# Optimization experiments

Measured on AMD Instinct MI355X. Metric: run time of the kernel, lower is better.

Reference implementation:

```python
import jax, jax.numpy as jnp
import numpy as np

N = 30000        # nodes
E = 150000       # edges
IN = 16          # in_feats
H = 32           # hidden_feats
C = 10           # num_classes


def setup_inputs() -> dict:
    key = jax.random.key(0)
    ks = jax.random.split(key, 11)
    s = 0.05
    return {
        "x": jax.random.normal(ks[0], (N, IN), jnp.float32),
        "edge_attr": jax.random.normal(ks[1], (E, 1), jnp.float32),
        "W1": jax.random.normal(ks[2], (1, IN * H), jnp.float32) * s,
        "b1": jax.random.normal(ks[3], (IN * H,), jnp.float32) * s,
        "W2": jax.random.normal(ks[4], (IN * H, IN * H), jnp.float32) * s,
        "b2": jax.random.normal(ks[5], (IN * H,), jnp.float32) * s,
        "root": jax.random.normal(ks[6], (IN, H), jnp.float32) * s,
        "bias1": jax.random.normal(ks[7], (H,), jnp.float32) * s,
        "Wg": jax.random.normal(ks[8], (H, C), jnp.float32) * s,
        "bg": jax.random.normal(ks[9], (C,), jnp.float32) * s,
        "edge_index": jax.random.randint(ks[10], (2, E), 0, N),
    }


def _forward(x, edge_attr, W1, b1, W2, b2, root, bias1, Wg, bg, edge_index):
    src, dst = edge_index[0], edge_index[1]

    # ---- NNConv: edge-MLP generates per-edge [IN, H] weight matrices ----
    h = jax.nn.relu(edge_attr @ W1 + b1)          # [E, IN*H]
    theta = (h @ W2 + b2).reshape(E, IN, H)       # [E, IN, H]
    msg = jnp.einsum('ei,eio->eo', x[src], theta)  # per-edge matvec [E, H]
    summed = jax.ops.segment_sum(msg, dst, num_segments=N)            # [N, H]
    cnt = jax.ops.segment_sum(jnp.ones((E,), x.dtype), dst, num_segments=N)
    aggr = summed / jnp.maximum(cnt, 1.0)[:, None]  # mean aggregation
    h1 = aggr + x @ root + bias1                    # root weight + bias
    h1 = jax.nn.relu(h1)
    # dropout skipped (eval mode)

    # ---- GCNConv with self-loops and symmetric normalization ----
    xw = h1 @ Wg                                   # [N, C]
    loop = jnp.arange(N)
    row = jnp.concatenate([src, loop])
    col = jnp.concatenate([dst, loop])
    deg = jax.ops.segment_sum(jnp.ones(row.shape, x.dtype), col, num_segments=N)
    dinv = jnp.where(deg > 0, jax.lax.rsqrt(jnp.maximum(deg, 1e-12)), 0.0)
    norm = dinv[row] * dinv[col]                   # [E+N]
    out = jax.ops.segment_sum(xw[row] * norm[:, None], col, num_segments=N) + bg

    return jax.nn.log_softmax(out, axis=1)


def reference(x, edge_attr, W1, b1, W2, b2, root, bias1, Wg, bg, edge_index):
    return _forward(x, edge_attr, W1, b1, W2, b2, root, bias1, Wg, bg, edge_index)
```

## Files before the change

### kernel.cpp

```cpp
#include <hip/hip_runtime.h>
#include <math.h>

#define N_NODES 30000
#define N_EDGES 150000
#define NB_E ((N_EDGES + 255) / 256)

__device__ __forceinline__ unsigned bf16_rne(float f) {
    unsigned u = __float_as_uint(f);
    u += 0x7FFFu + ((u >> 16) & 1u);
    return u >> 16;
}

__global__ void k1z_rank(const float* __restrict__ W1, const float* __restrict__ b1,
                         float* __restrict__ tsort, int* __restrict__ ksort,
                         int* __restrict__ deg) {
    __shared__ float st[512];
    int tid = threadIdx.x;
    float w = W1[tid], b = b1[tid];
    float t = (w != 0.0f) ? (-b / w) : 3.0e38f;
    st[tid] = t;
    __syncthreads();
    int rank = 0;
#pragma unroll 8
    for (int j = 0; j < 512; ++j) {
        float tj = st[j];
        rank += (tj < t || (tj == t && j < tid)) ? 1 : 0;
    }
    tsort[rank] = t;
    ksort[rank] = tid;
    int4* dz = (int4*)deg;
    for (int i = tid; i < N_NODES / 4; i += 512) dz[i] = make_int4(0, 0, 0, 0);
}

__global__ void __launch_bounds__(256) f2_prep(
        const int* __restrict__ ei, const float* __restrict__ ea,
        const float* __restrict__ tsort,
        int* __restrict__ deg, int* __restrict__ rankm,
        const float* __restrict__ W1, const float* __restrict__ b1,
        const float* __restrict__ W2, const int* __restrict__ ksort,
        float* __restrict__ PbA, float* __restrict__ PbB,
        float* __restrict__ SA, float* __restrict__ SB) {
    if (blockIdx.x < NB_E) {
        __shared__ float ts[512];
        for (int i = threadIdx.x; i < 512; i += 256) ts[i] = tsort[i];
        __syncthreads();
        int e = blockIdx.x * 256 + threadIdx.x;
        if (e >= N_EDGES) return;
        int rank = atomicAdd(&deg[ei[N_EDGES + e]], 1);
        float a = ea[e];
        int lo = 0, hi = 512;
        while (lo < hi) {
            int mid = (lo + hi) >> 1;
            if (ts[mid] < a) lo = mid + 1; else hi = mid;
        }
        rankm[e] = (rank << 10) | lo;
    } else {
        int bb = blockIdx.x - NB_E;
        int c = bb & 31;
        int jc = bb >> 5;
        int jt = jc * 256 + threadIdx.x;
        int jsrc = ((jt & 15) << 5) | (jt >> 4);
        float ba = 0.0f, bb2 = 0.0f, sa = 0.0f, sb = 0.0f;
#pragma unroll 4
        for (int s = 0; s < 16; ++s) {
            int k = c * 16 + s;
            float w = W1[k], b = b1[k];
            bool act = (w < 0.0f) || (w == 0.0f && b > 0.0f);
            if (act) {
                float w2 = W2[k * 512 + jsrc];
                ba = fmaf(w, w2, ba);
                bb2 = fmaf(b, w2, bb2);
            }
            int kr = ksort[c * 16 + s];
            float wr = W1[kr], br = b1[kr];
            float sgn = (wr > 0.0f) ? 1.0f : ((wr < 0.0f) ? -1.0f : 0.0f);
            float w2r = W2[kr * 512 + jsrc];
            sa = fmaf(sgn * wr, w2r, sa);
            sb = fmaf(sgn * br, w2r, sb);
        }
        PbA[c * 512 + jt] = ba; PbB[c * 512 + jt] = bb2;
        SA[c * 512 + jt] = sa;  SB[c * 512 + jt] = sb;
    }
}

__global__ void __launch_bounds__(1024) f3_scan_emit(
        const int* __restrict__ deg, int* __restrict__ offs,
        const float* __restrict__ W1, const float* __restrict__ b1,
        const float* __restrict__ b2, const float* __restrict__ W2,
        const int* __restrict__ ksort,
        const float* __restrict__ PbA, const float* __restrict__ PbB,
        const float* __restrict__ SA, const float* __restrict__ SB,
        unsigned int* __restrict__ T) {
    __shared__ int part[1024];
    if (blockIdx.x == 0) {
        int t = threadIdx.x;
        int base = t * 30;
        int loc[30];
        int s = 0;
#pragma unroll
        for (int i = 0; i < 30; ++i) {
            int idx = base + i;
            int v = (idx < N_NODES) ? deg[idx] : 0;
            loc[i] = v;
            s += v;
        }
        part[t] = s;
        __syncthreads();
        for (int off = 1; off < 1024; off <<= 1) {
            int v = part[t];
            int add = (t >= off) ? part[t - off] : 0;
            __syncthreads();
            part[t] = v + add;
            __syncthreads();
        }
        int run = (t > 0) ? part[t - 1] : 0;
#pragma unroll
        for (int i = 0; i < 30; ++i) {
            int idx = base + i;
            if (idx < N_NODES) offs[idx] = run;
            run += loc[i];
        }
        if (t == 1023) offs[N_NODES] = run;
    } else {
        int c = (blockIdx.x - 1) * 2 + (threadIdx.x >> 9);
        int jt = threadIdx.x & 511;
        int jsrc = ((jt & 15) << 5) | (jt >> 4);
        float runA = 0.0f, runB = 0.0f;
#pragma unroll
        for (int c2 = 0; c2 < 32; ++c2) {
            runA += PbA[c2 * 512 + jt];
            runB += PbB[c2 * 512 + jt];
            if (c2 < c) { runA += SA[c2 * 512 + jt]; runB += SB[c2 * 512 + jt]; }
        }
        float bb2 = b2[jsrc];
#pragma unroll 4
        for (int s = 0; s < 16; ++s) {
            int m = c * 16 + s;
            T[m * 512 + jt] = (bf16_rne(runA) << 16) | bf16_rne(runB + bb2);
            int k = ksort[m];
            float w = W1[k], b = b1[k];
            float sgn = (w > 0.0f) ? 1.0f : ((w < 0.0f) ? -1.0f : 0.0f);
            float w2 = W2[k * 512 + jsrc];
            runA = fmaf(sgn * w, w2, runA);
            runB = fmaf(sgn * b, w2, runB);
        }
        if (c == 31) {
            T[512 * 512 + jt] = (bf16_rne(runA) << 16) | bf16_rne(runB + bb2);
        }
    }
}

__global__ void __launch_bounds__(256) k3_edges(
        const float* __restrict__ x, const float* __restrict__ ea,
        const int* __restrict__ ei, const int* __restrict__ rankm,
        const int* __restrict__ offs, const unsigned int* __restrict__ T,
        unsigned short* __restrict__ msgbuf, int* __restrict__ ssrc) {
    int gid = blockIdx.x * blockDim.x + threadIdx.x;
    int lane = gid & 31;
    int g = gid >> 5;
    int e0 = g << 1;
    if (e0 >= N_EDGES) return;
    float2 aa = *(const float2*)(ea + e0);
    int2 ss = *(const int2*)(ei + e0);
    int2 dd = *(const int2*)(ei + N_EDGES + e0);
    int2 rr = *(const int2*)(rankm + e0);
    int m0 = rr.x & 1023, m1 = rr.y & 1023;
    int slot0 = offs[dd.x] + (rr.x >> 10);
    int slot1 = offs[dd.y] + (rr.y >> 10);
    const uint4* T0 = (const uint4*)(T + m0 * 512 + lane * 16);
    const uint4* T1 = (const uint4*)(T + m1 * 512 + lane * 16);
    uint4 p0 = T0[0], p1 = T0[1], p2 = T0[2], p3 = T0[3];
    uint4 q0 = T1[0], q1 = T1[1], q2 = T1[2], q3 = T1[3];
    float xv0 = (lane < 16) ? x[ss.x * 16 + lane] : 0.0f;
    float xv1 = (lane < 16) ? x[ss.y * 16 + lane] : 0.0f;
    float xa0 = 0.0f, xb0 = 0.0f, xa1 = 0.0f, xb1 = 0.0f;
    float xi;
#define STEP2(w0, w1, i)                                                   \
    xi = __shfl(xv0, i, 32);                                               \
    xa0 = fmaf(xi, __uint_as_float((w0) & 0xFFFF0000u), xa0);              \
    xb0 = fmaf(xi, __uint_as_float((w0) << 16), xb0);                      \
    xi = __shfl(xv1, i, 32);                                               \
    xa1 = fmaf(xi, __uint_as_float((w1) & 0xFFFF0000u), xa1);              \
    xb1 = fmaf(xi, __uint_as_float((w1) << 16), xb1);
    STEP2(p0.x, q0.x, 0)  STEP2(p0.y, q0.y, 1)  STEP2(p0.z, q0.z, 2)  STEP2(p0.w, q0.w, 3)
    STEP2(p1.x, q1.x, 4)  STEP2(p1.y, q1.y, 5)  STEP2(p1.z, q1.z, 6)  STEP2(p1.w, q1.w, 7)
    STEP2(p2.x, q2.x, 8)  STEP2(p2.y, q2.y, 9)  STEP2(p2.z, q2.z, 10) STEP2(p2.w, q2.w, 11)
    STEP2(p3.x, q3.x, 12) STEP2(p3.y, q3.y, 13) STEP2(p3.z, q3.z, 14) STEP2(p3.w, q3.w, 15)
#undef STEP2
    float msg0 = fmaf(aa.x, xa0, xb0);
    float msg1 = fmaf(aa.y, xa1, xb1);
    msgbuf[slot0 * 32 + lane] = (unsigned short)bf16_rne(msg0);
    msgbuf[slot1 * 32 + lane] = (unsigned short)bf16_rne(msg1);
    if (lane == 0) { ssrc[slot0] = ss.x; ssrc[slot1] = ss.y; }
}

__global__ void k4_nodes(const float* __restrict__ x, const int* __restrict__ offs,
                         const unsigned int* __restrict__ msgbuf,
                         const float* __restrict__ root, const float* __restrict__ bias1,
                         const float* __restrict__ Wg,
                         float* __restrict__ xw12) {
    __shared__ float sroot[512], sb1[32], swg[320];
    for (int i = threadIdx.x; i < 512; i += blockDim.x) sroot[i] = root[i];
    for (int i = threadIdx.x; i < 32; i += blockDim.x) sb1[i] = bias1[i];
    for (int i = threadIdx.x; i < 320; i += blockDim.x) swg[i] = Wg[i];
    __syncthreads();
    int n = blockIdx.x * blockDim.x + threadIdx.x;
    if (n >= N_NODES) return;
    int s0 = offs[n], s1 = offs[n + 1];
    float agg[32];
#pragma unroll
    for (int o = 0; o < 32; ++o) agg[o] = 0.0f;
    for (int sl = s0; sl < s1; ++sl) {
        const uint4* rp = (const uint4*)(msgbuf + sl * 16);
#pragma unroll
        for (int q = 0; q < 4; ++q) {
            uint4 v = rp[q];
            agg[q * 8 + 0] += __uint_as_float(v.x << 16);
            agg[q * 8 + 1] += __uint_as_float(v.x & 0xFFFF0000u);
            agg[q * 8 + 2] += __uint_as_float(v.y << 16);
            agg[q * 8 + 3] += __uint_as_float(v.y & 0xFFFF0000u);
            agg[q * 8 + 4] += __uint_as_float(v.z << 16);
            agg[q * 8 + 5] += __uint_as_float(v.z & 0xFFFF0000u);
            agg[q * 8 + 6] += __uint_as_float(v.w << 16);
            agg[q * 8 + 7] += __uint_as_float(v.w & 0xFFFF0000u);
        }
    }
    float c = (float)(s1 - s0);
    float inv = 1.0f / fmaxf(c, 1.0f);
    const float4* xp = (const float4*)(x + n * 16);
    float xr[16];
#pragma unroll
    for (int q = 0; q < 4; ++q) {
        float4 v = xp[q];
        xr[q * 4 + 0] = v.x; xr[q * 4 + 1] = v.y;
        xr[q * 4 + 2] = v.z; xr[q * 4 + 3] = v.w;
    }
    float acc[10];
#pragma unroll
    for (int cc = 0; cc < 10; ++cc) acc[cc] = 0.0f;
#pragma unroll
    for (int o = 0; o < 32; ++o) {
        float h = agg[o] * inv + sb1[o];
#pragma unroll
        for (int i = 0; i < 16; ++i) h = fmaf(xr[i], sroot[i * 32 + o], h);
        h = fmaxf(h, 0.0f);
#pragma unroll
        for (int cc = 0; cc < 10; ++cc) acc[cc] = fmaf(h, swg[o * 10 + cc], acc[cc]);
    }
    float4* op = (float4*)(xw12 + n * 12);
    op[0] = make_float4(acc[0], acc[1], acc[2], acc[3]);
    op[1] = make_float4(acc[4], acc[5], acc[6], acc[7]);
    op[2] = make_float4(acc[8], acc[9], rsqrtf(c + 1.0f), 0.0f);
}

__global__ void k56_final(const int* __restrict__ offs, const int* __restrict__ ssrc,
                          const float* __restrict__ xw12,
                          const float* __restrict__ bg, float* __restrict__ out) {
    __shared__ float sbg[16];
    if (threadIdx.x < 10) sbg[threadIdx.x] = bg[threadIdx.x];
    __syncthreads();
    int n = blockIdx.x * blockDim.x + threadIdx.x;
    if (n >= N_NODES) return;
    const float4* base = (const float4*)xw12;
    float4 r0 = base[n * 3], r1 = base[n * 3 + 1], r2 = base[n * 3 + 2];
    float dn = r2.z;
    float d2 = dn * dn;
    float acc[10];
    acc[0] = fmaf(r0.x, d2, sbg[0]); acc[1] = fmaf(r0.y, d2, sbg[1]);
    acc[2] = fmaf(r0.z, d2, sbg[2]); acc[3] = fmaf(r0.w, d2, sbg[3]);
    acc[4] = fmaf(r1.x, d2, sbg[4]); acc[5] = fmaf(r1.y, d2, sbg[5]);
    acc[6] = fmaf(r1.z, d2, sbg[6]); acc[7] = fmaf(r1.w, d2, sbg[7]);
    acc[8] = fmaf(r2.x, d2, sbg[8]); acc[9] = fmaf(r2.y, d2, sbg[9]);
    int s0 = offs[n], s1 = offs[n + 1];
    for (int sl = s0; sl < s1; ++sl) {
        int s = ssrc[sl];
        float4 q0 = base[s * 3], q1 = base[s * 3 + 1], q2 = base[s * 3 + 2];
        float nf = q2.z * dn;
        acc[0] = fmaf(q0.x, nf, acc[0]); acc[1] = fmaf(q0.y, nf, acc[1]);
        acc[2] = fmaf(q0.z, nf, acc[2]); acc[3] = fmaf(q0.w, nf, acc[3]);
        acc[4] = fmaf(q1.x, nf, acc[4]); acc[5] = fmaf(q1.y, nf, acc[5]);
        acc[6] = fmaf(q1.z, nf, acc[6]); acc[7] = fmaf(q1.w, nf, acc[7]);
        acc[8] = fmaf(q2.x, nf, acc[8]); acc[9] = fmaf(q2.y, nf, acc[9]);
    }
    float mx = -1e30f;
#pragma unroll
    for (int c = 0; c < 10; ++c) mx = fmaxf(mx, acc[c]);
    float se = 0.0f;
#pragma unroll
    for (int c = 0; c < 10; ++c) se += expf(acc[c] - mx);
    float lse = logf(se) + mx;
#pragma unroll
    for (int c = 0; c < 10; ++c) out[n * 10 + c] = acc[c] - lse;
}

extern "C" void kernel_launch(void* const* d_in, const int* in_sizes, int n_in,
                              void* d_out, int out_size, void* d_ws, size_t ws_size,
                              hipStream_t stream) {
    const float* x     = (const float*)d_in[0];
    const float* ea    = (const float*)d_in[1];
    const float* W1    = (const float*)d_in[2];
    const float* b1    = (const float*)d_in[3];
    const float* W2    = (const float*)d_in[4];
    const float* b2    = (const float*)d_in[5];
    const float* root  = (const float*)d_in[6];
    const float* bias1 = (const float*)d_in[7];
    const float* Wg    = (const float*)d_in[8];
    const float* bg    = (const float*)d_in[9];
    const int*   ei    = (const int*)d_in[10];
    float* out = (float*)d_out;

    unsigned int* T = (unsigned int*)d_ws;
    float* tsort  = (float*)(T + 513 * 512);
    int*   ksort  = (int*)(tsort + 512);
    unsigned short* msgbuf = (unsigned short*)(ksort + 512);
    int*   deg    = (int*)((float*)msgbuf + 2400000);
    int*   offs   = deg + N_NODES;
    int*   rankm  = offs + N_NODES + 4;
    int*   ssrc   = rankm + N_EDGES;
    float* xw12   = (float*)(ssrc + N_EDGES);
    float* PbA    = xw12 + N_NODES * 12;
    float* PbB    = PbA + 32 * 512;
    float* SA     = PbB + 32 * 512;
    float* SB     = SA + 32 * 512;

    k1z_rank<<<1, 512, 0, stream>>>(W1, b1, tsort, ksort, deg);
    f2_prep<<<NB_E + 64, 256, 0, stream>>>(ei, ea, tsort, deg, rankm,
                                           W1, b1, W2, ksort, PbA, PbB, SA, SB);
    f3_scan_emit<<<17, 1024, 0, stream>>>(deg, offs, W1, b1, b2, W2, ksort,
                                          PbA, PbB, SA, SB, T);
    k3_edges<<<(N_EDGES / 2 * 32 + 255) / 256, 256, 0, stream>>>(
        x, ea, ei, rankm, offs, T, msgbuf, ssrc);
    k4_nodes<<<(N_NODES + 255) / 256, 256, 0, stream>>>(x, offs,
                                                        (const unsigned int*)msgbuf,
                                                        root, bias1, Wg, xw12);
    k56_final<<<(N_NODES + 255) / 256, 256, 0, stream>>>(offs, ssrc, xw12, bg, out);
}
```

Baseline: 109.4 us.

## Parallelize node kernels across lanes: 32 lanes per node in k4, 8 in k56

k4_nodes now assigns one 32-lane group per node, with each lane owning one hidden feature. Lanes read messages coalesced, broadcast x by shuffles, and reduce the 10 class outputs with xor-shuffles. k56_final assigns 8 lanes per node, splits the neighbor gather across them, reduces by shuffle, and has lane 0 write the log-softmax with float2 stores. This targets the per-thread serial loops and poor memory coalescing of the one-thread-per-node versions, at the cost of many more threads and extra shuffle reductions.

```diff
diff --git a/kernel.cpp b/kernel.cpp
--- a/kernel.cpp
+++ b/kernel.cpp
@@ -194,85 +194,77 @@
     if (lane == 0) { ssrc[slot0] = ss.x; ssrc[slot1] = ss.y; }
 }
 
-__global__ void k4_nodes(const float* __restrict__ x, const int* __restrict__ offs,
-                         const unsigned int* __restrict__ msgbuf,
-                         const float* __restrict__ root, const float* __restrict__ bias1,
-                         const float* __restrict__ Wg,
-                         float* __restrict__ xw12) {
+__global__ void __launch_bounds__(256) k4_nodes(
+        const float* __restrict__ x, const int* __restrict__ offs,
+        const unsigned short* __restrict__ msgbuf,
+        const float* __restrict__ root, const float* __restrict__ bias1,
+        const float* __restrict__ Wg, float* __restrict__ xw12) {
     __shared__ float sroot[512], sb1[32], swg[320];
     for (int i = threadIdx.x; i < 512; i += blockDim.x) sroot[i] = root[i];
     for (int i = threadIdx.x; i < 32; i += blockDim.x) sb1[i] = bias1[i];
     for (int i = threadIdx.x; i < 320; i += blockDim.x) swg[i] = Wg[i];
     __syncthreads();
-    int n = blockIdx.x * blockDim.x + threadIdx.x;
+    int gid = blockIdx.x * blockDim.x + threadIdx.x;
+    int lane = gid & 31;
+    int n = gid >> 5;
     if (n >= N_NODES) return;
     int s0 = offs[n], s1 = offs[n + 1];
-    float agg[32];
-#pragma unroll
-    for (int o = 0; o < 32; ++o) agg[o] = 0.0f;
+    float agg = 0.0f;
     for (int sl = s0; sl < s1; ++sl) {
-        const uint4* rp = (const uint4*)(msgbuf + sl * 16);
-#pragma unroll
-        for (int q = 0; q < 4; ++q) {
-            uint4 v = rp[q];
-            agg[q * 8 + 0] += __uint_as_float(v.x << 16);
-            agg[q * 8 + 1] += __uint_as_float(v.x & 0xFFFF0000u);
-            agg[q * 8 + 2] += __uint_as_float(v.y << 16);
-            agg[q * 8 + 3] += __uint_as_float(v.y & 0xFFFF0000u);
-            agg[q * 8 + 4] += __uint_as_float(v.z << 16);
-            agg[q * 8 + 5] += __uint_as_float(v.z & 0xFFFF0000u);
-            agg[q * 8 + 6] += __uint_as_float(v.w << 16);
-            agg[q * 8 + 7] += __uint_as_float(v.w & 0xFFFF0000u);
-        }
+        unsigned short v = msgbuf[sl * 32 + lane];
+        agg += __uint_as_float(((unsigned)v) << 16);
     }
     float c = (float)(s1 - s0);
     float inv = 1.0f / fmaxf(c, 1.0f);
-    const float4* xp = (const float4*)(x + n * 16);
-    float xr[16];
-#pragma unroll
-    for (int q = 0; q < 4; ++q) {
-        float4 v = xp[q];
-        xr[q * 4 + 0] = v.x; xr[q * 4 + 1] = v.y;
-        xr[q * 4 + 2] = v.z; xr[q * 4 + 3] = v.w;
-    }
-    float acc[10];
-#pragma unroll
-    for (int cc = 0; cc < 10; ++cc) acc[cc] = 0.0f;
-#pragma unroll
-    for (int o = 0; o < 32; ++o) {
-        float h = agg[o] * inv + sb1[o];
-#pragma unroll
-        for (int i = 0; i < 16; ++i) h = fmaf(xr[i], sroot[i * 32 + o], h);
-        h = fmaxf(h, 0.0f);
-#pragma unroll
-        for (int cc = 0; cc < 10; ++cc) acc[cc] = fmaf(h, swg[o * 10 + cc], acc[cc]);
+    float xv = (lane < 16) ? x[n * 16 + lane] : 0.0f;
+    float h = fmaf(agg, inv, sb1[lane]);
+    float xi;
+#pragma unroll
+    for (int i = 0; i < 16; ++i) {
+        xi = __shfl(xv, i, 32);
+        h = fmaf(xi, sroot[i * 32 + lane], h);
+    }
+    h = fmaxf(h, 0.0f);
+    float p[10];
+#pragma unroll
+    for (int cc = 0; cc < 10; ++cc) p[cc] = h * swg[lane * 10 + cc];
+#pragma unroll
+    for (int st = 1; st < 32; st <<= 1) {
+#pragma unroll
+        for (int cc = 0; cc < 10; ++cc) p[cc] += __shfl_xor(p[cc], st, 32);
     }
     float4* op = (float4*)(xw12 + n * 12);
-    op[0] = make_float4(acc[0], acc[1], acc[2], acc[3]);
-    op[1] = make_float4(acc[4], acc[5], acc[6], acc[7]);
-    op[2] = make_float4(acc[8], acc[9], rsqrtf(c + 1.0f), 0.0f);
-}
-
-__global__ void k56_final(const int* __restrict__ offs, const int* __restrict__ ssrc,
-                          const float* __restrict__ xw12,
-                          const float* __restrict__ bg, float* __restrict__ out) {
+    if (lane == 0) op[0] = make_float4(p[0], p[1], p[2], p[3]);
+    else if (lane == 1) op[1] = make_float4(p[4], p[5], p[6], p[7]);
+    else if (lane == 2) op[2] = make_float4(p[8], p[9], rsqrtf(c + 1.0f), 0.0f);
+}
+
+__global__ void __launch_bounds__(256) k56_final(
+        const int* __restrict__ offs, const int* __restrict__ ssrc,
+        const float* __restrict__ xw12, const float* __restrict__ bg,
+        float* __restrict__ out) {
     __shared__ float sbg[16];
     if (threadIdx.x < 10) sbg[threadIdx.x] = bg[threadIdx.x];
     __syncthreads();
-    int n = blockIdx.x * blockDim.x + threadIdx.x;
+    int gid = blockIdx.x * blockDim.x + threadIdx.x;
+    int lane = gid & 7;
+    int n = gid >> 3;
     if (n >= N_NODES) return;
     const float4* base = (const float4*)xw12;
-    float4 r0 = base[n * 3], r1 = base[n * 3 + 1], r2 = base[n * 3 + 2];
-    float dn = r2.z;
-    float d2 = dn * dn;
+    float dn = xw12[n * 12 + 10];
     float acc[10];
-    acc[0] = fmaf(r0.x, d2, sbg[0]); acc[1] = fmaf(r0.y, d2, sbg[1]);
-    acc[2] = fmaf(r0.z, d2, sbg[2]); acc[3] = fmaf(r0.w, d2, sbg[3]);
-    acc[4] = fmaf(r1.x, d2, sbg[4]); acc[5] = fmaf(r1.y, d2, sbg[5]);
-    acc[6] = fmaf(r1.z, d2, sbg[6]); acc[7] = fmaf(r1.w, d2, sbg[7]);
-    acc[8] = fmaf(r2.x, d2, sbg[8]); acc[9] = fmaf(r2.y, d2, sbg[9]);
+#pragma unroll
+    for (int cc = 0; cc < 10; ++cc) acc[cc] = 0.0f;
+    if (lane == 0) {
+        float4 r0 = base[n * 3], r1 = base[n * 3 + 1], r2 = base[n * 3 + 2];
+        float d2 = dn * dn;
+        acc[0] = r0.x * d2; acc[1] = r0.y * d2; acc[2] = r0.z * d2;
+        acc[3] = r0.w * d2; acc[4] = r1.x * d2; acc[5] = r1.y * d2;
+        acc[6] = r1.z * d2; acc[7] = r1.w * d2; acc[8] = r2.x * d2;
+        acc[9] = r2.y * d2;
+    }
     int s0 = offs[n], s1 = offs[n + 1];
-    for (int sl = s0; sl < s1; ++sl) {
+    for (int sl = s0 + lane; sl < s1; sl += 8) {
         int s = ssrc[sl];
         float4 q0 = base[s * 3], q1 = base[s * 3 + 1], q2 = base[s * 3 + 2];
         float nf = q2.z * dn;
@@ -282,15 +274,26 @@
         acc[6] = fmaf(q1.z, nf, acc[6]); acc[7] = fmaf(q1.w, nf, acc[7]);
         acc[8] = fmaf(q2.x, nf, acc[8]); acc[9] = fmaf(q2.y, nf, acc[9]);
     }
-    float mx = -1e30f;
-#pragma unroll
-    for (int c = 0; c < 10; ++c) mx = fmaxf(mx, acc[c]);
-    float se = 0.0f;
-#pragma unroll
-    for (int c = 0; c < 10; ++c) se += expf(acc[c] - mx);
-    float lse = logf(se) + mx;
-#pragma unroll
-    for (int c = 0; c < 10; ++c) out[n * 10 + c] = acc[c] - lse;
+#pragma unroll
+    for (int st = 1; st < 8; st <<= 1) {
+#pragma unroll
+        for (int cc = 0; cc < 10; ++cc) acc[cc] += __shfl_xor(acc[cc], st, 8);
+    }
+    if (lane == 0) {
+        float mx = -1e30f;
+#pragma unroll
+        for (int cc = 0; cc < 10; ++cc) { acc[cc] += sbg[cc]; mx = fmaxf(mx, acc[cc]); }
+        float se = 0.0f;
+#pragma unroll
+        for (int cc = 0; cc < 10; ++cc) se += expf(acc[cc] - mx);
+        float lse = logf(se) + mx;
+        float2* o2 = (float2*)(out + n * 10);
+        o2[0] = make_float2(acc[0] - lse, acc[1] - lse);
+        o2[1] = make_float2(acc[2] - lse, acc[3] - lse);
+        o2[2] = make_float2(acc[4] - lse, acc[5] - lse);
+        o2[3] = make_float2(acc[6] - lse, acc[7] - lse);
+        o2[4] = make_float2(acc[8] - lse, acc[9] - lse);
+    }
 }
 
 extern "C" void kernel_launch(void* const* d_in, const int* in_sizes, int n_in,
@@ -330,8 +333,8 @@
                                           PbA, PbB, SA, SB, T);
     k3_edges<<<(N_EDGES / 2 * 32 + 255) / 256, 256, 0, stream>>>(
         x, ea, ei, rankm, offs, T, msgbuf, ssrc);
-    k4_nodes<<<(N_NODES + 255) / 256, 256, 0, stream>>>(x, offs,
-                                                        (const unsigned int*)msgbuf,
-                                                        root, bias1, Wg, xw12);
-    k56_final<<<(N_NODES + 255) / 256, 256, 0, stream>>>(offs, ssrc, xw12, bg, out);
-}
+    k4_nodes<<<(N_NODES * 32 + 255) / 256, 256, 0, stream>>>(
+        x, offs, msgbuf, root, bias1, Wg, xw12);
+    k56_final<<<(N_NODES * 8 + 255) / 256, 256, 0, stream>>>(offs, ssrc, xw12,
+                                                             bg, out);
+}
```

New measurement: 112.6 us. 1.03x slower.

## Aggregate edge messages with float atomics instead of a sorted bf16 message buffer

Applied to the files above, without the earlier changes.

The edge kernel now adds each fp32 message directly into a per-node summed buffer with atomicAdd, replacing the bf16 messages written to CSR slots that the node kernel then reduced. The node kernel reads 32 summed floats per node instead of looping over its slots. The rank kernel gets extra blocks that zero the summed buffer and the degree array together. This avoids the scattered message writes and the per-node gather loop, at the cost of up to 4.8M global float atomics with contention on busy nodes and a non-deterministic summation order.

```diff
diff --git a/kernel.cpp b/kernel.cpp
--- a/kernel.cpp
+++ b/kernel.cpp
@@ -13,23 +13,29 @@
 
 __global__ void k1z_rank(const float* __restrict__ W1, const float* __restrict__ b1,
                          float* __restrict__ tsort, int* __restrict__ ksort,
-                         int* __restrict__ deg) {
-    __shared__ float st[512];
-    int tid = threadIdx.x;
-    float w = W1[tid], b = b1[tid];
-    float t = (w != 0.0f) ? (-b / w) : 3.0e38f;
-    st[tid] = t;
-    __syncthreads();
-    int rank = 0;
+                         int* __restrict__ zbase ) {
+    if (blockIdx.x == 0) {
+        __shared__ float st[512];
+        int tid = threadIdx.x;
+        float w = W1[tid], b = b1[tid];
+        float t = (w != 0.0f) ? (-b / w) : 3.0e38f;
+        st[tid] = t;
+        __syncthreads();
+        int rank = 0;
 #pragma unroll 8
-    for (int j = 0; j < 512; ++j) {
-        float tj = st[j];
-        rank += (tj < t || (tj == t && j < tid)) ? 1 : 0;
-    }
-    tsort[rank] = t;
-    ksort[rank] = tid;
-    int4* dz = (int4*)deg;
-    for (int i = tid; i < N_NODES / 4; i += 512) dz[i] = make_int4(0, 0, 0, 0);
+        for (int j = 0; j < 512; ++j) {
+            float tj = st[j];
+            rank += (tj < t || (tj == t && j < tid)) ? 1 : 0;
+        }
+        tsort[rank] = t;
+        ksort[rank] = tid;
+    } else {
+        int4* dz = (int4*)zbase;
+        const int n4 = N_NODES * 33 / 4;
+        int4 z = make_int4(0, 0, 0, 0);
+        for (int i = (blockIdx.x - 1) * 512 + threadIdx.x; i < n4; i += 31 * 512)
+            dz[i] = z;
+    }
 }
 
 __global__ void __launch_bounds__(256) f2_prep(
@@ -154,7 +160,7 @@
         const float* __restrict__ x, const float* __restrict__ ea,
         const int* __restrict__ ei, const int* __restrict__ rankm,
         const int* __restrict__ offs, const unsigned int* __restrict__ T,
-        unsigned short* __restrict__ msgbuf, int* __restrict__ ssrc) {
+        float* __restrict__ summed, int* __restrict__ ssrc) {
     int gid = blockIdx.x * blockDim.x + threadIdx.x;
     int lane = gid & 31;
     int g = gid >> 5;
@@ -165,8 +171,6 @@
     int2 dd = *(const int2*)(ei + N_EDGES + e0);
     int2 rr = *(const int2*)(rankm + e0);
     int m0 = rr.x & 1023, m1 = rr.y & 1023;
-    int slot0 = offs[dd.x] + (rr.x >> 10);
-    int slot1 = offs[dd.y] + (rr.y >> 10);
     const uint4* T0 = (const uint4*)(T + m0 * 512 + lane * 16);
     const uint4* T1 = (const uint4*)(T + m1 * 512 + lane * 16);
     uint4 p0 = T0[0], p1 = T0[1], p2 = T0[2], p3 = T0[3];
@@ -189,13 +193,16 @@
 #undef STEP2
     float msg0 = fmaf(aa.x, xa0, xb0);
     float msg1 = fmaf(aa.y, xa1, xb1);
-    msgbuf[slot0 * 32 + lane] = (unsigned short)bf16_rne(msg0);
-    msgbuf[slot1 * 32 + lane] = (unsigned short)bf16_rne(msg1);
-    if (lane == 0) { ssrc[slot0] = ss.x; ssrc[slot1] = ss.y; }
+    atomicAdd(&summed[dd.x * 32 + lane], msg0);
+    atomicAdd(&summed[dd.y * 32 + lane], msg1);
+    if (lane == 0) {
+        ssrc[offs[dd.x] + (rr.x >> 10)] = ss.x;
+        ssrc[offs[dd.y] + (rr.y >> 10)] = ss.y;
+    }
 }
 
 __global__ void k4_nodes(const float* __restrict__ x, const int* __restrict__ offs,
-                         const unsigned int* __restrict__ msgbuf,
+                         const float* __restrict__ summed,
                          const float* __restrict__ root, const float* __restrict__ bias1,
                          const float* __restrict__ Wg,
                          float* __restrict__ xw12) {
@@ -206,26 +213,7 @@
     __syncthreads();
     int n = blockIdx.x * blockDim.x + threadIdx.x;
     if (n >= N_NODES) return;
-    int s0 = offs[n], s1 = offs[n + 1];
-    float agg[32];
-#pragma unroll
-    for (int o = 0; o < 32; ++o) agg[o] = 0.0f;
-    for (int sl = s0; sl < s1; ++sl) {
-        const uint4* rp = (const uint4*)(msgbuf + sl * 16);
-#pragma unroll
-        for (int q = 0; q < 4; ++q) {
-            uint4 v = rp[q];
-            agg[q * 8 + 0] += __uint_as_float(v.x << 16);
-            agg[q * 8 + 1] += __uint_as_float(v.x & 0xFFFF0000u);
-            agg[q * 8 + 2] += __uint_as_float(v.y << 16);
-            agg[q * 8 + 3] += __uint_as_float(v.y & 0xFFFF0000u);
-            agg[q * 8 + 4] += __uint_as_float(v.z << 16);
-            agg[q * 8 + 5] += __uint_as_float(v.z & 0xFFFF0000u);
-            agg[q * 8 + 6] += __uint_as_float(v.w << 16);
-            agg[q * 8 + 7] += __uint_as_float(v.w & 0xFFFF0000u);
-        }
-    }
-    float c = (float)(s1 - s0);
+    float c = (float)(offs[n + 1] - offs[n]);
     float inv = 1.0f / fmaxf(c, 1.0f);
     const float4* xp = (const float4*)(x + n * 16);
     float xr[16];
@@ -235,12 +223,20 @@
         xr[q * 4 + 0] = v.x; xr[q * 4 + 1] = v.y;
         xr[q * 4 + 2] = v.z; xr[q * 4 + 3] = v.w;
     }
+    const float4* sp = (const float4*)(summed + n * 32);
+    float sm[32];
+#pragma unroll
+    for (int q = 0; q < 8; ++q) {
+        float4 v = sp[q];
+        sm[q * 4 + 0] = v.x; sm[q * 4 + 1] = v.y;
+        sm[q * 4 + 2] = v.z; sm[q * 4 + 3] = v.w;
+    }
     float acc[10];
 #pragma unroll
     for (int cc = 0; cc < 10; ++cc) acc[cc] = 0.0f;
 #pragma unroll
     for (int o = 0; o < 32; ++o) {
-        float h = agg[o] * inv + sb1[o];
+        float h = sm[o] * inv + sb1[o];
 #pragma unroll
         for (int i = 0; i < 16; ++i) h = fmaf(xr[i], sroot[i * 32 + o], h);
         h = fmaxf(h, 0.0f);
@@ -312,8 +308,8 @@
     unsigned int* T = (unsigned int*)d_ws;
     float* tsort  = (float*)(T + 513 * 512);
     int*   ksort  = (int*)(tsort + 512);
-    unsigned short* msgbuf = (unsigned short*)(ksort + 512);
-    int*   deg    = (int*)((float*)msgbuf + 2400000);
+    float* summed = (float*)(ksort + 512);
+    int*   deg    = (int*)(summed + N_NODES * 32);
     int*   offs   = deg + N_NODES;
     int*   rankm  = offs + N_NODES + 4;
     int*   ssrc   = rankm + N_EDGES;
@@ -323,15 +319,14 @@
     float* SA     = PbB + 32 * 512;
     float* SB     = SA + 32 * 512;
 
-    k1z_rank<<<1, 512, 0, stream>>>(W1, b1, tsort, ksort, deg);
+    k1z_rank<<<32, 512, 0, stream>>>(W1, b1, tsort, ksort, (int*)summed);
     f2_prep<<<NB_E + 64, 256, 0, stream>>>(ei, ea, tsort, deg, rankm,
                                            W1, b1, W2, ksort, PbA, PbB, SA, SB);
     f3_scan_emit<<<17, 1024, 0, stream>>>(deg, offs, W1, b1, b2, W2, ksort,
                                           PbA, PbB, SA, SB, T);
     k3_edges<<<(N_EDGES / 2 * 32 + 255) / 256, 256, 0, stream>>>(
-        x, ea, ei, rankm, offs, T, msgbuf, ssrc);
-    k4_nodes<<<(N_NODES + 255) / 256, 256, 0, stream>>>(x, offs,
-                                                        (const unsigned int*)msgbuf,
+        x, ea, ei, rankm, offs, T, summed, ssrc);
+    k4_nodes<<<(N_NODES + 255) / 256, 256, 0, stream>>>(x, offs, summed,
                                                         root, bias1, Wg, xw12);
     k56_final<<<(N_NODES + 255) / 256, 256, 0, stream>>>(offs, ssrc, xw12, bg, out);
 }
```

Measured after the change: 105.3 us (median of 3 runs). 3.8% less time.
